# Kernel optimization log

Measured on AMD Instinct MI355X. Metric: run time of the kernel, lower is better.

Reference implementation:

```python
import jax, jax.numpy as jnp
import numpy as np

N = 100000   # num_nodes
D = 128      # hidden_dim
E = 640000   # num_edges


def setup_inputs() -> dict:
    key = jax.random.key(0)
    k0, k1, k2, k3 = jax.random.split(key, 4)
    node_features = jax.random.normal(k0, (N, D), dtype=jnp.float32) * 0.02
    # GCNConv linear weights (glorot-style scale), bias initialized to zero
    scale = 1.0 / np.sqrt(D)
    W1 = jax.random.normal(k1, (D, D), dtype=jnp.float32) * scale
    b1 = jnp.zeros((D,), dtype=jnp.float32)
    W2 = jax.random.normal(k2, (D, D), dtype=jnp.float32) * scale
    b2 = jnp.zeros((D,), dtype=jnp.float32)
    edge_index = jax.random.randint(k3, (2, E), 0, N, dtype=jnp.int32)
    return {"node_features": node_features, "W1": W1, "b1": b1,
            "W2": W2, "b2": b2, "edge_index": edge_index}


def gcn_layer(x, W, b, row, col):
    # PyG GCNConv: linear (no bias) -> symmetric norm deg^-1/2 -> scatter-add -> +bias
    x = x @ W.T                                   # [N, D]
    ones = jnp.ones(row.shape, dtype=x.dtype)
    deg = jax.ops.segment_sum(ones, col, num_segments=N)   # in-degree incl. self-loops
    dis = jnp.where(deg > 0, jax.lax.rsqrt(deg), 0.0)       # deg_inv_sqrt, inf -> 0
    norm = dis[row] * dis[col]                    # [E_tot]
    msgs = norm[:, None] * x[row]                 # gather + scale, [E_tot, D]
    out = jax.ops.segment_sum(msgs, col, num_segments=N)    # scatter-aggregate
    return out + b


def reference(node_features, W1, b1, W2, b2, edge_index):
    # add self-loops once (GCNConv does this per call; same result since graph is static)
    loops = jnp.arange(N, dtype=edge_index.dtype)
    row = jnp.concatenate([edge_index[0], loops])
    col = jnp.concatenate([edge_index[1], loops])
    x = jax.nn.relu(gcn_layer(node_features, W1, b1, row, col))
    x = jax.nn.relu(gcn_layer(x, W2, b2, row, col))
    return x
```

## Files before the change

kernel.cpp:

```cpp
#include <hip/hip_runtime.h>

#define DD 128

typedef short bf16x8 __attribute__((ext_vector_type(8)));
typedef float f32x4 __attribute__((ext_vector_type(4)));

__device__ __forceinline__ unsigned short f2bf(float f) {
    unsigned int u = __builtin_bit_cast(unsigned int, f);
    u += 0x7fffu + ((u >> 16) & 1u);
    return (unsigned short)(u >> 16);
}
__device__ __forceinline__ float bflo(unsigned int u) { return __builtin_bit_cast(float, u << 16); }
__device__ __forceinline__ float bfhi(unsigned int u) { return __builtin_bit_cast(float, u & 0xffff0000u); }

__global__ __launch_bounds__(256) void k_part(const int* __restrict__ cnt,
                                              int* __restrict__ part, int n) {
    __shared__ int s[256];
    int t = threadIdx.x;
    int i = blockIdx.x * 256 + t;
    s[t] = (i < n) ? cnt[i] : 0;
    __syncthreads();
    for (int off = 128; off > 0; off >>= 1) {
        if (t < off) s[t] += s[t + off];
        __syncthreads();
    }
    if (t == 0) part[blockIdx.x] = s[0];
}

__global__ __launch_bounds__(256) void k_apply(const int* __restrict__ cnt,
                                               const int* __restrict__ part,
                                               int* __restrict__ rowptr,
                                               int* __restrict__ cursor,
                                               float* __restrict__ dis, int n) {
    __shared__ int s[256];
    __shared__ int sbase;
    int t = threadIdx.x;
    int bid = blockIdx.x;

    int a = 0;
    for (int j = t; j < bid; j += 256) a += part[j];
    s[t] = a;
    __syncthreads();
    for (int off = 128; off > 0; off >>= 1) {
        if (t < off) s[t] += s[t + off];
        __syncthreads();
    }
    if (t == 0) sbase = s[0];
    __syncthreads();

    int i = bid * 256 + t;
    int c = (i < n) ? cnt[i] : 0;
    s[t] = c;
    __syncthreads();
    for (int off = 1; off < 256; off <<= 1) {
        int u = (t >= off) ? s[t - off] : 0;
        __syncthreads();
        s[t] += u;
        __syncthreads();
    }
    int base = sbase + s[t] - c;
    if (i < n) {
        rowptr[i] = base;
        cursor[i] = base;
        dis[i] = rsqrtf((float)c + 1.0f);
        if (i == n - 1) rowptr[n] = base + c;
    }
}

__global__ void k_permute(const int* __restrict__ row, const int* __restrict__ col,
                          int* __restrict__ cursor, int* __restrict__ srow, int E) {
    int e = blockIdx.x * blockDim.x + threadIdx.x;
    if (e >= E) return;
    int p = atomicAdd(&cursor[col[e]], 1);
    srow[p] = row[e];
}

__global__ __launch_bounds__(512) void k_gemm_mfma(const float* __restrict__ Xv,
                                                   const float* __restrict__ W,
                                                   unsigned short* __restrict__ Y,
                                                   int nrows, int gemm_blocks,
                                                   const int* __restrict__ ecol,
                                                   int* __restrict__ cnt, int E) {
    __shared__ unsigned short Ws[128 * 128];
    const int t = threadIdx.x;

    if ((int)blockIdx.x >= gemm_blocks) {
        int e = (blockIdx.x - gemm_blocks) * 512 + t;
        if (e < E) atomicAdd(&cnt[ecol[e]], 1);
        return;
    }

    #pragma unroll
    for (int i = 0; i < 4; ++i) {
        int g  = i * 512 + t;
        int wr = g >> 4, ch = g & 15;
        const float* src = W + wr * 128 + ch * 8;
        float4 f0 = *(const float4*)src;
        float4 f1 = *(const float4*)(src + 4);
        unsigned short u[8] = { f2bf(f0.x), f2bf(f0.y), f2bf(f0.z), f2bf(f0.w),
                                f2bf(f1.x), f2bf(f1.y), f2bf(f1.z), f2bf(f1.w) };
        int dst = wr * 128 + ((ch ^ (wr & 15)) << 3);
        *(uint4*)&Ws[dst] = *(const uint4*)u;
    }

    const int wid  = t >> 6;
    const int lane = t & 63;
    const int lr   = lane & 15;
    const int lk   = lane >> 4;
    const long base = (long)blockIdx.x * 128;

    long arow = base + wid * 16 + lr;
    bool rowok = arow < nrows;
    if (!rowok) arow = nrows - 1;

    float4 a[8];
    #pragma unroll
    for (int kc = 0; kc < 4; ++kc) {
        const float* ap = Xv + arow * 128 + kc * 32 + lk * 8;
        a[2 * kc]     = *(const float4*)ap;
        a[2 * kc + 1] = *(const float4*)(ap + 4);
    }
    __syncthreads();

    f32x4 acc[8] = {};
    #pragma unroll
    for (int kc = 0; kc < 4; ++kc) {
        bf16x8 af;
        af[0] = (short)f2bf(a[2*kc].x);   af[1] = (short)f2bf(a[2*kc].y);
        af[2] = (short)f2bf(a[2*kc].z);   af[3] = (short)f2bf(a[2*kc].w);
        af[4] = (short)f2bf(a[2*kc+1].x); af[5] = (short)f2bf(a[2*kc+1].y);
        af[6] = (short)f2bf(a[2*kc+1].z); af[7] = (short)f2bf(a[2*kc+1].w);
        #pragma unroll
        for (int jt = 0; jt < 8; ++jt) {
            int j  = jt * 16 + lr;
            int ch = (kc * 4 + lk) ^ lr;
            const bf16x8* bp = (const bf16x8*)&Ws[j * 128 + (ch << 3)];
            acc[jt] = __builtin_amdgcn_mfma_f32_16x16x32_bf16(*bp, af, acc[jt], 0, 0, 0);
        }
    }

    if (rowok) {
        unsigned short* yp = Y + arow * 128 + lk * 4;
        #pragma unroll
        for (int jt = 0; jt < 8; ++jt) {
            unsigned int d0 = (unsigned int)f2bf(acc[jt][0]) | ((unsigned int)f2bf(acc[jt][1]) << 16);
            unsigned int d1 = (unsigned int)f2bf(acc[jt][2]) | ((unsigned int)f2bf(acc[jt][3]) << 16);
            uint2 u; u.x = d0; u.y = d1;
            *(uint2*)(yp + jt * 16) = u;
        }
    }
}

__device__ __forceinline__ void fma8(float* acc, float nm, uint4 q) {
    acc[0] += nm * bflo(q.x); acc[1] += nm * bfhi(q.x);
    acc[2] += nm * bflo(q.y); acc[3] += nm * bfhi(q.y);
    acc[4] += nm * bflo(q.z); acc[5] += nm * bfhi(q.z);
    acc[6] += nm * bflo(q.w); acc[7] += nm * bfhi(q.w);
}

__device__ __forceinline__ void agg_node(const int* __restrict__ rowptr,
                                         const int* __restrict__ srow,
                                         const float* __restrict__ dis,
                                         const unsigned short* __restrict__ xw,
                                         const float* __restrict__ b,
                                         long v, int c, float* o) {
    float dv = dis[v], s = dv * dv;
    float acc[8] = {};
    fma8(acc, s, *(const uint4*)(xw + v * 128 + c));

    int e0 = rowptr[v], e1 = rowptr[v + 1];
    int nfull = (e1 - e0) >> 2;
    int e = e0;
    if (nfull) {
        int r0 = srow[e], r1 = srow[e + 1], r2 = srow[e + 2], r3 = srow[e + 3];
        for (int bi = 1; bi < nfull; ++bi) {
            int eb = e0 + bi * 4;
            int p0 = srow[eb], p1 = srow[eb + 1], p2 = srow[eb + 2], p3 = srow[eb + 3];
            float n0 = dis[r0] * dv, n1 = dis[r1] * dv;
            float n2 = dis[r2] * dv, n3 = dis[r3] * dv;
            uint4 q0 = *(const uint4*)(xw + (long)r0 * 128 + c);
            uint4 q1 = *(const uint4*)(xw + (long)r1 * 128 + c);
            uint4 q2 = *(const uint4*)(xw + (long)r2 * 128 + c);
            uint4 q3 = *(const uint4*)(xw + (long)r3 * 128 + c);
            fma8(acc, n0, q0); fma8(acc, n1, q1);
            fma8(acc, n2, q2); fma8(acc, n3, q3);
            r0 = p0; r1 = p1; r2 = p2; r3 = p3;
        }
        float n0 = dis[r0] * dv, n1 = dis[r1] * dv;
        float n2 = dis[r2] * dv, n3 = dis[r3] * dv;
        uint4 q0 = *(const uint4*)(xw + (long)r0 * 128 + c);
        uint4 q1 = *(const uint4*)(xw + (long)r1 * 128 + c);
        uint4 q2 = *(const uint4*)(xw + (long)r2 * 128 + c);
        uint4 q3 = *(const uint4*)(xw + (long)r3 * 128 + c);
        fma8(acc, n0, q0); fma8(acc, n1, q1);
        fma8(acc, n2, q2); fma8(acc, n3, q3);
        e = e0 + nfull * 4;
    }
    for (; e < e1; ++e) {
        int   r1 = srow[e];
        float n1 = dis[r1] * dv;
        fma8(acc, n1, *(const uint4*)(xw + (long)r1 * 128 + c));
    }

    float4 b0 = *(const float4*)(b + c);
    float4 b1 = *(const float4*)(b + c + 4);
    o[0] = fmaxf(acc[0] + b0.x, 0.0f); o[1] = fmaxf(acc[1] + b0.y, 0.0f);
    o[2] = fmaxf(acc[2] + b0.z, 0.0f); o[3] = fmaxf(acc[3] + b0.w, 0.0f);
    o[4] = fmaxf(acc[4] + b1.x, 0.0f); o[5] = fmaxf(acc[5] + b1.y, 0.0f);
    o[6] = fmaxf(acc[6] + b1.z, 0.0f); o[7] = fmaxf(acc[7] + b1.w, 0.0f);
}

__global__ __launch_bounds__(512) void k_agg_gemm(const int* __restrict__ rowptr,
                                                  const int* __restrict__ srow,
                                                  const float* __restrict__ dis,
                                                  const unsigned short* __restrict__ xw,
                                                  const float* __restrict__ b1,
                                                  const float* __restrict__ W2,
                                                  unsigned short* __restrict__ Y,
                                                  int n) {
    __shared__ unsigned short Ws[128 * 128];
    __shared__ unsigned short Hs[64 * 128];
    const int t = threadIdx.x;

    #pragma unroll
    for (int i = 0; i < 4; ++i) {
        int g  = i * 512 + t;
        int wr = g >> 4, ch = g & 15;
        const float* src = W2 + wr * 128 + ch * 8;
        float4 f0 = *(const float4*)src;
        float4 f1 = *(const float4*)(src + 4);
        unsigned short u[8] = { f2bf(f0.x), f2bf(f0.y), f2bf(f0.z), f2bf(f0.w),
                                f2bf(f1.x), f2bf(f1.y), f2bf(f1.z), f2bf(f1.w) };
        int dst = wr * 128 + ((ch ^ (wr & 15)) << 3);
        *(uint4*)&Ws[dst] = *(const uint4*)u;
    }

    const long nb = (long)blockIdx.x * 64;
    const int c  = (t & 15) * 8;
    #pragma unroll
    for (int pass = 0; pass < 2; ++pass) {
        int  lrow = pass * 32 + (t >> 4);
        long v    = nb + lrow;
        float o[8] = {};
        if (v < n) agg_node(rowptr, srow, dis, xw, b1, v, c, o);
        unsigned int pk[4];
        pk[0] = (unsigned int)f2bf(o[0]) | ((unsigned int)f2bf(o[1]) << 16);
        pk[1] = (unsigned int)f2bf(o[2]) | ((unsigned int)f2bf(o[3]) << 16);
        pk[2] = (unsigned int)f2bf(o[4]) | ((unsigned int)f2bf(o[5]) << 16);
        pk[3] = (unsigned int)f2bf(o[6]) | ((unsigned int)f2bf(o[7]) << 16);
        int ch = (t & 15) ^ (lrow & 15);
        *(uint4*)&Hs[lrow * 128 + (ch << 3)] = *(const uint4*)pk;
    }
    __syncthreads();

    const int wid  = t >> 6;
    const int lane = t & 63;
    const int lr   = lane & 15;
    const int lk   = lane >> 4;
    const int rw   = wid & 3;
    const int jb   = (wid >> 2) * 4;
    const int wrow = rw * 16 + lr;

    f32x4 acc[4] = {};
    #pragma unroll
    for (int kc = 0; kc < 4; ++kc) {
        int ach = (kc * 4 + lk) ^ (wrow & 15);
        bf16x8 af = *(const bf16x8*)&Hs[wrow * 128 + (ach << 3)];
        #pragma unroll
        for (int j4 = 0; j4 < 4; ++j4) {
            int j  = (jb + j4) * 16 + lr;
            int ch = (kc * 4 + lk) ^ lr;
            const bf16x8* bp = (const bf16x8*)&Ws[j * 128 + (ch << 3)];
            acc[j4] = __builtin_amdgcn_mfma_f32_16x16x32_bf16(*bp, af, acc[j4], 0, 0, 0);
        }
    }

    long grow = nb + wrow;
    if (grow < n) {
        unsigned short* yp = Y + grow * 128 + lk * 4;
        #pragma unroll
        for (int j4 = 0; j4 < 4; ++j4) {
            unsigned int d0 = (unsigned int)f2bf(acc[j4][0]) | ((unsigned int)f2bf(acc[j4][1]) << 16);
            unsigned int d1 = (unsigned int)f2bf(acc[j4][2]) | ((unsigned int)f2bf(acc[j4][3]) << 16);
            uint2 u; u.x = d0; u.y = d1;
            *(uint2*)(yp + (jb + j4) * 16) = u;
        }
    }
}

__global__ __launch_bounds__(256) void k_agg_out(const int* __restrict__ rowptr,
                                                 const int* __restrict__ srow,
                                                 const float* __restrict__ dis,
                                                 const unsigned short* __restrict__ xw,
                                                 const float* __restrict__ b,
                                                 float* __restrict__ out, int n) {
    long v = blockIdx.x * 16 + (threadIdx.x >> 4);
    if (v >= n) return;
    int c = (threadIdx.x & 15) * 8;
    float o[8];
    agg_node(rowptr, srow, dis, xw, b, v, c, o);
    float* op = out + v * 128 + c;
    *(float4*)op       = make_float4(o[0], o[1], o[2], o[3]);
    *(float4*)(op + 4) = make_float4(o[4], o[5], o[6], o[7]);
}

extern "C" void kernel_launch(void* const* d_in, const int* in_sizes, int n_in,
                              void* d_out, int out_size, void* d_ws, size_t ws_size,
                              hipStream_t stream) {
    const float* X  = (const float*)d_in[0];
    const float* W1 = (const float*)d_in[1];
    const float* b1 = (const float*)d_in[2];
    const float* W2 = (const float*)d_in[3];
    const float* b2 = (const float*)d_in[4];
    const int*   ei = (const int*)d_in[5];
    const int N = in_sizes[0] / DD;
    const int E = in_sizes[5] / 2;
    const int* row = ei;
    const int* col = ei + E;

    char* p = (char*)d_ws;
    auto carve = [&](size_t bytes) { char* q = p; p += (bytes + 255) & ~(size_t)255; return q; };
    int*            cnt    = (int*)           carve((size_t)N * 4);
    int*            rowptr = (int*)           carve((size_t)(N + 1) * 4);
    int*            cursor = (int*)           carve((size_t)N * 4);
    int*            part   = (int*)           carve(1024 * 4);
    int*            srow   = (int*)           carve((size_t)E * 4);
    float*          dis    = (float*)         carve((size_t)N * 4);
    unsigned short* xw     = (unsigned short*)carve((size_t)N * DD * 2);
    unsigned short* xw2    = (unsigned short*)carve((size_t)N * DD * 2);

    const int NBLK = (N + 255) / 256;
    const int gemm_grid = (N + 127) / 128;
    const int aggg_grid = (N + 63) / 64;
    const int edge_grid = (E + 511) / 512;
    const int aggo_grid = (N + 15) / 16;

    hipMemsetAsync(cnt, 0, (size_t)N * 4, stream);
    k_gemm_mfma<<<gemm_grid + edge_grid, 512, 0, stream>>>(
        X, W1, xw, N, gemm_grid, col, cnt, E);

    k_part<<<NBLK, 256, 0, stream>>>(cnt, part, N);
    k_apply<<<NBLK, 256, 0, stream>>>(cnt, part, rowptr, cursor, dis, N);
    k_permute<<<(E + 255) / 256, 256, 0, stream>>>(row, col, cursor, srow, E);

    k_agg_gemm<<<aggg_grid, 512, 0, stream>>>(rowptr, srow, dis, xw, b1, W2, xw2, N);

    k_agg_out<<<aggo_grid, 256, 0, stream>>>(rowptr, srow, dis, xw2, b2, (float*)d_out, N);
}
```

Measured before the change: 170.4 us.

## Record per-edge rank from degree atomics and drop the partial-sum kernel

The atomicAdd return value from the degree-counting pass is now stored as a per-edge rank, so the permute step computes each edge's slot as rowptr plus rank without a second round of atomics. This removes the cursor array and its atomics. The separate block-partial-sum kernel is also removed: each scan block now sums every cnt entry before its own range directly. That saves a launch but adds quadratic global reads, since late blocks read up to N counts each, and the per-edge rank array costs extra writes and reads of E ints.

After: 196.4 us. +15.3%, slower.

```diff
diff --git a/kernel.cpp b/kernel.cpp
--- a/kernel.cpp
+++ b/kernel.cpp
@@ -13,32 +13,17 @@
 __device__ __forceinline__ float bflo(unsigned int u) { return __builtin_bit_cast(float, u << 16); }
 __device__ __forceinline__ float bfhi(unsigned int u) { return __builtin_bit_cast(float, u & 0xffff0000u); }
 
-__global__ __launch_bounds__(256) void k_part(const int* __restrict__ cnt,
-                                              int* __restrict__ part, int n) {
-    __shared__ int s[256];
-    int t = threadIdx.x;
-    int i = blockIdx.x * 256 + t;
-    s[t] = (i < n) ? cnt[i] : 0;
-    __syncthreads();
-    for (int off = 128; off > 0; off >>= 1) {
-        if (t < off) s[t] += s[t + off];
-        __syncthreads();
-    }
-    if (t == 0) part[blockIdx.x] = s[0];
-}
-
 __global__ __launch_bounds__(256) void k_apply(const int* __restrict__ cnt,
-                                               const int* __restrict__ part,
                                                int* __restrict__ rowptr,
-                                               int* __restrict__ cursor,
                                                float* __restrict__ dis, int n) {
     __shared__ int s[256];
     __shared__ int sbase;
     int t = threadIdx.x;
     int bid = blockIdx.x;
+    int lim = bid * 256;
 
     int a = 0;
-    for (int j = t; j < bid; j += 256) a += part[j];
+    for (int j = t; j < lim; j += 256) a += cnt[j];
     s[t] = a;
     __syncthreads();
     for (int off = 128; off > 0; off >>= 1) {
@@ -48,7 +33,7 @@
     if (t == 0) sbase = s[0];
     __syncthreads();
 
-    int i = bid * 256 + t;
+    int i = lim + t;
     int c = (i < n) ? cnt[i] : 0;
     s[t] = c;
     __syncthreads();
@@ -61,17 +46,17 @@
     int base = sbase + s[t] - c;
     if (i < n) {
         rowptr[i] = base;
-        cursor[i] = base;
         dis[i] = rsqrtf((float)c + 1.0f);
         if (i == n - 1) rowptr[n] = base + c;
     }
 }
 
 __global__ void k_permute(const int* __restrict__ row, const int* __restrict__ col,
-                          int* __restrict__ cursor, int* __restrict__ srow, int E) {
+                          const int* __restrict__ rowptr, const int* __restrict__ rank,
+                          int* __restrict__ srow, int E) {
     int e = blockIdx.x * blockDim.x + threadIdx.x;
     if (e >= E) return;
-    int p = atomicAdd(&cursor[col[e]], 1);
+    int p = rowptr[col[e]] + rank[e];
     srow[p] = row[e];
 }
 
@@ -80,13 +65,17 @@
                                                    unsigned short* __restrict__ Y,
                                                    int nrows, int gemm_blocks,
                                                    const int* __restrict__ ecol,
-                                                   int* __restrict__ cnt, int E) {
+                                                   int* __restrict__ cnt,
+                                                   int* __restrict__ rank, int E) {
     __shared__ unsigned short Ws[128 * 128];
     const int t = threadIdx.x;
 
     if ((int)blockIdx.x >= gemm_blocks) {
         int e = (blockIdx.x - gemm_blocks) * 512 + t;
-        if (e < E) atomicAdd(&cnt[ecol[e]], 1);
+        if (e < E) {
+            int r = atomicAdd(&cnt[ecol[e]], 1);
+            rank[e] = r;
+        }
         return;
     }
 
@@ -322,8 +311,7 @@
     auto carve = [&](size_t bytes) { char* q = p; p += (bytes + 255) & ~(size_t)255; return q; };
     int*            cnt    = (int*)           carve((size_t)N * 4);
     int*            rowptr = (int*)           carve((size_t)(N + 1) * 4);
-    int*            cursor = (int*)           carve((size_t)N * 4);
-    int*            part   = (int*)           carve(1024 * 4);
+    int*            rank   = (int*)           carve((size_t)E * 4);
     int*            srow   = (int*)           carve((size_t)E * 4);
     float*          dis    = (float*)         carve((size_t)N * 4);
     unsigned short* xw     = (unsigned short*)carve((size_t)N * DD * 2);
@@ -337,11 +325,10 @@
 
     hipMemsetAsync(cnt, 0, (size_t)N * 4, stream);
     k_gemm_mfma<<<gemm_grid + edge_grid, 512, 0, stream>>>(
-        X, W1, xw, N, gemm_grid, col, cnt, E);
-
-    k_part<<<NBLK, 256, 0, stream>>>(cnt, part, N);
-    k_apply<<<NBLK, 256, 0, stream>>>(cnt, part, rowptr, cursor, dis, N);
-    k_permute<<<(E + 255) / 256, 256, 0, stream>>>(row, col, cursor, srow, E);
+        X, W1, xw, N, gemm_grid, col, cnt, rank, E);
+
+    k_apply<<<NBLK, 256, 0, stream>>>(cnt, rowptr, dis, N);
+    k_permute<<<(E + 255) / 256, 256, 0, stream>>>(row, col, rowptr, rank, srow, E);
 
     k_agg_gemm<<<aggg_grid, 512, 0, stream>>>(rowptr, srow, dis, xw, b1, W2, xw2, N);
 
```
